# Kernel tuning notes

Hardware: AMD Instinct MI355X
Metric: run time of the kernel (lower is better)

## Reference

```python
import jax, jax.numpy as jnp
import numpy as np

N_NODES = 50000


def gcn_conv(x, edge_index, W, b, n_nodes):
    # PyG GCNConv: h = D^{-1/2} (A + I) D^{-1/2} (x @ W) + b
    loops = jnp.arange(n_nodes, dtype=edge_index.dtype)
    src = jnp.concatenate([edge_index[0], loops])
    dst = jnp.concatenate([edge_index[1], loops])
    deg = jax.ops.segment_sum(jnp.ones_like(dst, dtype=x.dtype), dst,
                              num_segments=n_nodes)
    dinv = jnp.where(deg > 0, jax.lax.rsqrt(deg), 0.0)
    norm = dinv[src] * dinv[dst]                      # [E+N]
    h = x @ W                                          # [N, out]
    msg = h[src] * norm[:, None]                       # gather + scale
    out = jax.ops.segment_sum(msg, dst, num_segments=n_nodes)
    return out + b


def setup_inputs() -> dict:
    key = jax.random.key(0)
    ks = jax.random.split(key, 8)
    in_c, hid_c, out_c = 256, 128, 64
    x = jax.random.normal(ks[0], (N_NODES, in_c), dtype=jnp.float32)
    edge_index = jax.random.randint(ks[1], (2, 800000), 0, N_NODES, dtype=jnp.int64)
    pos_edge_index = jax.random.randint(ks[2], (2, 200000), 0, N_NODES, dtype=jnp.int64)
    neg_edge_index = jax.random.randint(ks[3], (2, 200000), 0, N_NES if False else N_NODES, dtype=jnp.int64)
    W1 = jax.random.normal(ks[4], (in_c, hid_c), dtype=jnp.float32) / np.sqrt(in_c)
    b1 = jnp.zeros((hid_c,), dtype=jnp.float32)
    W2 = jax.random.normal(ks[5], (hid_c, out_c), dtype=jnp.float32) / np.sqrt(hid_c)
    b2 = jnp.zeros((out_c,), dtype=jnp.float32)
    return {"x": x, "edge_index": edge_index, "pos_edge_index": pos_edge_index,
            "neg_edge_index": neg_edge_index, "W1": W1, "b1": b1, "W2": W2, "b2": b2}


def reference(x, edge_index, pos_edge_index, neg_edge_index, W1, b1, W2, b2):
    n = x.shape[0]
    h = jax.nn.relu(gcn_conv(x, edge_index, W1, b1, n))
    z = gcn_conv(h, edge_index, W2, b2, n)             # [N, out_c]
    ei = jnp.concatenate([pos_edge_index, neg_edge_index], axis=-1)
    logits = jnp.sum(z[ei[0]] * z[ei[1]], axis=-1)     # [E_pos + E_neg]
    return logits
```

## Files before the change

### kernel.cpp

```cpp
#include <hip/hip_runtime.h>
#include <stdint.h>

constexpr int N_NODES = 50000;
constexpr int E_EDGES = 800000;
constexpr int E_PAIR  = 200000;
constexpr int C_IN    = 256;
constexpr int C_HID   = 128;
constexpr int C_OUT   = 64;
constexpr int SLOT    = 64;

constexpr int NBUCK = 49;
constexpr int BCAP  = 18432;
constexpr int CHUNK = 2048;

typedef __attribute__((ext_vector_type(8))) short bf8_t;
typedef __attribute__((ext_vector_type(4))) float f32x4;

__device__ inline void bf_split(float v, uint32_t& hi16, uint32_t& lo16) {
    union { float f; uint32_t u; } c; c.f = v;
    hi16 = c.u >> 16;
    union { uint32_t u; float f; } h; h.u = hi16 << 16;
    float r = v - h.f;
    union { float f; uint32_t u; } rr; rr.f = r;
    lo16 = rr.u >> 16;
}

__device__ inline uint16_t f2bf(float f) {
    union { float f; uint32_t u; } c; c.f = f;
    uint32_t u = c.u + 0x7fff + ((c.u >> 16) & 1);
    return (uint16_t)(u >> 16);
}
__device__ inline uint32_t pack2bf(float a, float b) {
    union { float f; uint32_t u; } ca, cb; ca.f = a; cb.f = b;
    uint32_t ua = ca.u + 0x7fff + ((ca.u >> 16) & 1);
    uint32_t ub = cb.u + 0x7fff + ((cb.u >> 16) & 1);
    return (ua >> 16) | ((ub >> 16) << 16);
}
__device__ inline void acc_bf8(float* a, uint4 v) {
    const uint32_t p[4] = {v.x, v.y, v.z, v.w};
#pragma unroll
    for (int i = 0; i < 4; ++i) {
        union { uint32_t u; float f; } lo, hi;
        lo.u = p[i] << 16; hi.u = p[i] & 0xffff0000u;
        a[2 * i]     += lo.f;
        a[2 * i + 1] += hi.f;
    }
}
__device__ inline float dot_bf8(uint4 a, uint4 b) {
    const uint32_t pa[4] = {a.x, a.y, a.z, a.w};
    const uint32_t pb[4] = {b.x, b.y, b.z, b.w};
    float v = 0.f;
#pragma unroll
    for (int i = 0; i < 4; ++i) {
        union { uint32_t u; float f; } al, ah, bl, bh;
        al.u = pa[i] << 16; ah.u = pa[i] & 0xffff0000u;
        bl.u = pb[i] << 16; bh.u = pb[i] & 0xffff0000u;
        v += al.f * bl.f + ah.f * bh.f;
    }
    return v;
}

__global__ __launch_bounds__(256) void binA_kernel(
        const int* __restrict__ src, const int* __restrict__ dst,
        int* __restrict__ gcur, uint32_t* __restrict__ ebuf) {
    __shared__ int cnt[NBUCK], loc[NBUCK], lim[NBUCK], abase[NBUCK], wcur[NBUCK];
    __shared__ uint32_t stag[CHUNK];
    __shared__ uint8_t  bof[CHUNK];

    const int t  = threadIdx.x;
    const int e0 = blockIdx.x * CHUNK;
    const int n  = min(CHUNK, E_EDGES - e0);

    if (t < NBUCK) cnt[t] = 0;
    __syncthreads();

    uint32_t pk[CHUNK / 256]; int bk[CHUNK / 256];
    int ne = 0;
    for (int j = t; j < n; j += 256) {
        int d = dst[e0 + j], s = src[e0 + j];
        int b = d >> 10;
        pk[ne] = ((uint32_t)(d & 1023) << 16) | (uint32_t)s;
        bk[ne] = b;
        atomicAdd(&cnt[b], 1);
        ++ne;
    }
    __syncthreads();
    if (t == 0) {
        int run = 0;
        for (int b = 0; b < NBUCK; ++b) { loc[b] = run; run += cnt[b]; }
    }
    __syncthreads();
    if (t < NBUCK) {
        int base = atomicAdd(&gcur[t], cnt[t]);
        int room = BCAP - base; if (room < 0) room = 0;
        lim[t]   = loc[t] + room;
        abase[t] = t * BCAP + base - loc[t];
        wcur[t]  = loc[t];
    }
    __syncthreads();
#pragma unroll
    for (int i = 0; i < CHUNK / 256; ++i) {
        if (i < ne) {
            int p = atomicAdd(&wcur[bk[i]], 1);
            stag[p] = pk[i];
            bof[p]  = (uint8_t)bk[i];
        }
    }
    __syncthreads();
    for (int j = t; j < n; j += 256) {
        int b = bof[j];
        if (j < lim[b]) ebuf[abase[b] + j] = stag[j];
    }
}

__global__ __launch_bounds__(1024) void binB_kernel(
        const int* __restrict__ gcur, const uint32_t* __restrict__ ebuf,
        uint16_t* __restrict__ col2, int* __restrict__ degc,
        float* __restrict__ dinv) {
    __shared__ int cur[1024];
    const int t = threadIdx.x;
    const int b = blockIdx.x;
    cur[t] = 0;
    __syncthreads();

    int cn = gcur[b]; if (cn > BCAP) cn = BCAP;
    const uint32_t* eb = ebuf + (size_t)b * BCAP;
    const size_t nbase = (size_t)b << 10;

    int j = t;
    for (; j + 3 * 1024 < cn; j += 4 * 1024) {
        uint32_t v0 = eb[j], v1 = eb[j + 1024], v2 = eb[j + 2048], v3 = eb[j + 3072];
        int p0 = atomicAdd(&cur[v0 >> 16], 1);
        int p1 = atomicAdd(&cur[v1 >> 16], 1);
        int p2 = atomicAdd(&cur[v2 >> 16], 1);
        int p3 = atomicAdd(&cur[v3 >> 16], 1);
        if (p0 < SLOT) col2[((nbase + (v0 >> 16)) << 6) + p0] = (uint16_t)(v0 & 0xffff);
        if (p1 < SLOT) col2[((nbase + (v1 >> 16)) << 6) + p1] = (uint16_t)(v1 & 0xffff);
        if (p2 < SLOT) col2[((nbase + (v2 >> 16)) << 6) + p2] = (uint16_t)(v2 & 0xffff);
        if (p3 < SLOT) col2[((nbase + (v3 >> 16)) << 6) + p3] = (uint16_t)(v3 & 0xffff);
    }
    for (; j < cn; j += 1024) {
        uint32_t v = eb[j];
        int p = atomicAdd(&cur[v >> 16], 1);
        if (p < SLOT) col2[((nbase + (v >> 16)) << 6) + p] = (uint16_t)(v & 0xffff);
    }
    __syncthreads();
    int node = (int)nbase + t;
    if (node < N_NODES) {
        int dg = cur[t];
        degc[node] = dg;
        dinv[node] = rsqrtf((float)dg + 1.0f);
    }
}

template<int K, int N>
__global__ void wprep_kernel(const float* __restrict__ W, uint16_t* __restrict__ swz) {
    int id = blockIdx.x * blockDim.x + threadIdx.x;
    if (id >= K * N) return;
    int k = id / N, n = id & (N - 1);
    uint32_t h, l; bf_split(W[id], h, l);
    int c = k >> 5, kq = (k >> 3) & 3, kk = k & 7, ct = n >> 4, nn = n & 15;
    int idx = (((c * (N / 16) + ct) * 4 + kq) * 16 + nn) * 8 + kk;
    swz[idx]         = (uint16_t)h;
    swz[K * N + idx] = (uint16_t)l;
}

template<int K, int N>
__global__ __launch_bounds__(256, 3) void gemm_mfma_kernel(
        const float* __restrict__ A, const uint16_t* __restrict__ Bswz,
        const float* __restrict__ dinv, uint16_t* __restrict__ out, int M) {
    constexpr int BM = 64, BK = 32;
    constexpr int CT   = N / 32;
    constexpr int NSUB = N / 16;
    constexpr int ABYTES = BM * BK * 2;
    constexpr int BBYTES = NSUB * 1024;
    __shared__ char sm[2 * ABYTES + 2 * BBYTES];
    char* As_hi = sm;
    char* As_lo = sm + ABYTES;
    char* Bs_hi = sm + 2 * ABYTES;
    char* Bs_lo = sm + 2 * ABYTES + BBYTES;

    const int t    = threadIdx.x;
    const int lane = t & 63;
    const int w    = t >> 6;
    const int wrow = w & 1, wcol = w >> 1;
    const int m0   = blockIdx.x * BM;

    const int sr = t >> 2, skq = t & 3;
    int arow = m0 + sr; if (arow > M - 1) arow = M - 1;
    const float* aptr = A + (size_t)arow * K + skq * 8;
    const int aslot = ((sr >> 4) * 64 + skq * 16 + (sr & 15)) * 16;

    f32x4 acc[2][CT];
#pragma unroll
    for (int rt = 0; rt < 2; ++rt)
#pragma unroll
        for (int ct = 0; ct < CT; ++ct) {
            f32x4 z = {0.f, 0.f, 0.f, 0.f};
            acc[rt][ct] = z;
        }

    const uint4* gh = (const uint4*)Bswz;
    const uint4* gl = (const uint4*)(Bswz + (size_t)K * N);

    constexpr int NCH = K / BK;
#pragma unroll 1
    for (int c = 0; c < NCH; ++c) {
        float4 v0 = *(const float4*)(aptr + c * BK);
        float4 v1 = *(const float4*)(aptr + c * BK + 4);
        uint4 bh0, bl0, bh1, bl1;
        {
            const uint4* ch = gh + (size_t)c * (BBYTES / 16);
            const uint4* cl = gl + (size_t)c * (BBYTES / 16);
            bh0 = ch[t]; bl0 = cl[t];
            if constexpr (NSUB == 8) { bh1 = ch[t + 256]; bl1 = cl[t + 256]; }
        }
        __syncthreads();
        {
            float e[8] = {v0.x, v0.y, v0.z, v0.w, v1.x, v1.y, v1.z, v1.w};
            uint32_t hp[4], lp[4];
#pragma unroll
            for (int j = 0; j < 4; ++j) {
                uint32_t h0, l0, h1, l1;
                bf_split(e[2 * j],     h0, l0);
                bf_split(e[2 * j + 1], h1, l1);
                hp[j] = h0 | (h1 << 16);
                lp[j] = l0 | (l1 << 16);
            }
            *(uint4*)(As_hi + aslot) = make_uint4(hp[0], hp[1], hp[2], hp[3]);
            *(uint4*)(As_lo + aslot) = make_uint4(lp[0], lp[1], lp[2], lp[3]);
        }
        *(uint4*)(Bs_hi + t * 16) = bh0;
        *(uint4*)(Bs_lo + t * 16) = bl0;
        if constexpr (NSUB == 8) {
            *(uint4*)(Bs_hi + (t + 256) * 16) = bh1;
            *(uint4*)(Bs_lo + (t + 256) * 16) = bl1;
        }
        __syncthreads();
        bf8_t Ah[2], Al[2];
#pragma unroll
        for (int rt = 0; rt < 2; ++rt) {
            int st = wrow * 2 + rt;
            Ah[rt] = *(const bf8_t*)(As_hi + st * 1024 + lane * 16);
            Al[rt] = *(const bf8_t*)(As_lo + st * 1024 + lane * 16);
        }
#pragma unroll
        for (int ct = 0; ct < CT; ++ct) {
            int cg = wcol * CT + ct;
            bf8_t Bh = *(const bf8_t*)(Bs_hi + cg * 1024 + lane * 16);
            bf8_t Bl = *(const bf8_t*)(Bs_lo + cg * 1024 + lane * 16);
#pragma unroll
            for (int rt = 0; rt < 2; ++rt) {
                acc[rt][ct] = __builtin_amdgcn_mfma_f32_16x16x32_bf16(Ah[rt], Bh, acc[rt][ct], 0, 0, 0);
                acc[rt][ct] = __builtin_amdgcn_mfma_f32_16x16x32_bf16(Ah[rt], Bl, acc[rt][ct], 0, 0, 0);
                acc[rt][ct] = __builtin_amdgcn_mfma_f32_16x16x32_bf16(Al[rt], Bh, acc[rt][ct], 0, 0, 0);
            }
        }
    }

#pragma unroll
    for (int rt = 0; rt < 2; ++rt) {
        int rowbase = m0 + wrow * 32 + rt * 16 + (lane >> 4) * 4;
#pragma unroll
        for (int ct = 0; ct < CT; ++ct) {
            int n = (wcol * CT + ct) * 16 + (lane & 15);
#pragma unroll
            for (int r = 0; r < 4; ++r) {
                int m = rowbase + r;
                if (m < M) out[(size_t)m * N + n] = f2bf(acc[rt][ct][r] * dinv[m]);
            }
        }
    }
}

__global__ __launch_bounds__(256, 3) void gemm_a16_kernel(
        const uint16_t* __restrict__ A, const uint16_t* __restrict__ Bswz,
        const float* __restrict__ dinv, uint16_t* __restrict__ out, int M) {
    constexpr int K = 128, N = 64, BM = 64, BK = 32;
    constexpr int CT = 2;
    constexpr int ABYTES = 4096, BBYTES = 4096;
    __shared__ char sm[ABYTES + 2 * BBYTES];
    char* As    = sm;
    char* Bs_hi = sm + ABYTES;
    char* Bs_lo = sm + ABYTES + BBYTES;

    const int t    = threadIdx.x;
    const int lane = t & 63;
    const int w    = t >> 6;
    const int wrow = w & 1, wcol = w >> 1;
    const int m0   = blockIdx.x * BM;

    const int sr = t >> 2, skq = t & 3;
    int arow = m0 + sr; if (arow > M - 1) arow = M - 1;
    const uint16_t* aptr = A + (size_t)arow * K + skq * 8;
    const int aslot = ((sr >> 4) * 64 + skq * 16 + (sr & 15)) * 16;

    f32x4 acc[2][CT];
#pragma unroll
    for (int rt = 0; rt < 2; ++rt)
#pragma unroll
        for (int ct = 0; ct < CT; ++ct) {
            f32x4 z = {0.f, 0.f, 0.f, 0.f};
            acc[rt][ct] = z;
        }

    const uint4* gh = (const uint4*)Bswz;
    const uint4* gl = (const uint4*)(Bswz + (size_t)K * N);

    constexpr int NCH = K / BK;
#pragma unroll 1
    for (int c = 0; c < NCH; ++c) {
        uint4 av  = *(const uint4*)(aptr + c * BK);
        uint4 bh0 = gh[(size_t)c * 256 + t];
        uint4 bl0 = gl[(size_t)c * 256 + t];
        __syncthreads();
        *(uint4*)(As + aslot)    = av;
        *(uint4*)(Bs_hi + t * 16) = bh0;
        *(uint4*)(Bs_lo + t * 16) = bl0;
        __syncthreads();
        bf8_t Ah[2];
#pragma unroll
        for (int rt = 0; rt < 2; ++rt)
            Ah[rt] = *(const bf8_t*)(As + (wrow * 2 + rt) * 1024 + lane * 16);
#pragma unroll
        for (int ct = 0; ct < CT; ++ct) {
            int cg = wcol * CT + ct;
            bf8_t Bh = *(const bf8_t*)(Bs_hi + cg * 1024 + lane * 16);
            bf8_t Bl = *(const bf8_t*)(Bs_lo + cg * 1024 + lane * 16);
#pragma unroll
            for (int rt = 0; rt < 2; ++rt) {
                acc[rt][ct] = __builtin_amdgcn_mfma_f32_16x16x32_bf16(Ah[rt], Bh, acc[rt][ct], 0, 0, 0);
                acc[rt][ct] = __builtin_amdgcn_mfma_f32_16x16x32_bf16(Ah[rt], Bl, acc[rt][ct], 0, 0, 0);
            }
        }
    }

#pragma unroll
    for (int rt = 0; rt < 2; ++rt) {
        int rowbase = m0 + wrow * 32 + rt * 16 + (lane >> 4) * 4;
#pragma unroll
        for (int ct = 0; ct < CT; ++ct) {
            int n = (wcol * CT + ct) * 16 + (lane & 15);
#pragma unroll
            for (int r = 0; r < 4; ++r) {
                int m = rowbase + r;
                if (m < M) out[(size_t)m * N + n] = f2bf(acc[rt][ct][r] * dinv[m]);
            }
        }
    }
}

template<int F, bool RELU>
__global__ __launch_bounds__(256) void gather_kernel(
        const uint16_t* __restrict__ col2, const int* __restrict__ degc,
        const uint16_t* __restrict__ hs, const float* __restrict__ dinv,
        const float* __restrict__ bias, uint16_t* __restrict__ out) {
    constexpr int LPN = F / 8;
    constexpr int NPW = 64 / LPN;
    const int lane = threadIdx.x & 63;
    const int sub  = lane / LPN;
    const int l    = lane % LPN;
    const int node = blockIdx.x * (4 * NPW) + (threadIdx.x >> 6) * NPW + sub;
    if (node >= N_NODES) return;

    int dg = degc[node]; if (dg > SLOT) dg = SLOT;
    const uint4* hs4 = (const uint4*)hs;

    float a0[8], a1[8];
    {
        uint4 self = hs4[(size_t)node * LPN + l];
#pragma unroll
        for (int i = 0; i < 8; ++i) { a0[i] = 0.f; a1[i] = 0.f; }
        acc_bf8(a0, self);
    }
    const int base = node * SLOT;

    for (int c = 0; c * LPN < dg; ++c) {
        int cnt = dg - c * LPN; if (cnt > LPN) cnt = LPN;
        int cv = (l < cnt) ? (int)col2[base + c * LPN + l] : 0;
        int j = 0;
        for (; j + 4 <= cnt; j += 4) {
            int s0 = __shfl(cv, sub * LPN + j,     64);
            int s1 = __shfl(cv, sub * LPN + j + 1, 64);
            int s2 = __shfl(cv, sub * LPN + j + 2, 64);
            int s3 = __shfl(cv, sub * LPN + j + 3, 64);
            uint4 v0 = hs4[(size_t)s0 * LPN + l];
            uint4 v1 = hs4[(size_t)s1 * LPN + l];
            uint4 v2 = hs4[(size_t)s2 * LPN + l];
            uint4 v3 = hs4[(size_t)s3 * LPN + l];
            acc_bf8(a0, v0); acc_bf8(a1, v1);
            acc_bf8(a0, v2); acc_bf8(a1, v3);
        }
        for (; j < cnt; ++j) {
            int s = __shfl(cv, sub * LPN + j, 64);
            uint4 v = hs4[(size_t)s * LPN + l];
            acc_bf8(a0, v);
        }
    }

    const float dn = dinv[node];
    float4 bb0 = ((const float4*)bias)[2 * l];
    float4 bb1 = ((const float4*)bias)[2 * l + 1];
    float o[8];
    o[0] = (a0[0] + a1[0]) * dn + bb0.x;
    o[1] = (a0[1] + a1[1]) * dn + bb0.y;
    o[2] = (a0[2] + a1[2]) * dn + bb0.z;
    o[3] = (a0[3] + a1[3]) * dn + bb0.w;
    o[4] = (a0[4] + a1[4]) * dn + bb1.x;
    o[5] = (a0[5] + a1[5]) * dn + bb1.y;
    o[6] = (a0[6] + a1[6]) * dn + bb1.z;
    o[7] = (a0[7] + a1[7]) * dn + bb1.w;
    if (RELU) {
#pragma unroll
        for (int i = 0; i < 8; ++i) o[i] = fmaxf(o[i], 0.f);
    }
    uint4 res = make_uint4(pack2bf(o[0], o[1]), pack2bf(o[2], o[3]),
                           pack2bf(o[4], o[5]), pack2bf(o[6], o[7]));
    ((uint4*)out)[(size_t)node * LPN + l] = res;
}

__global__ __launch_bounds__(256) void logits_kernel(
        const int* __restrict__ pos, const int* __restrict__ neg,
        const uint16_t* __restrict__ z, float* __restrict__ out) {
    const int t = threadIdx.x;
    const int l = t & 7;
    const int e = (blockIdx.x * 256 + t) >> 3;
    if (e >= 2 * E_PAIR) return;
    int s, d;
    if (e < E_PAIR) { s = pos[e];          d = pos[E_PAIR + e]; }
    else            { s = neg[e - E_PAIR]; d = neg[e];          }
    const uint4* z4 = (const uint4*)z;
    uint4 ua = z4[(size_t)s * 8 + l];
    uint4 ub = z4[(size_t)d * 8 + l];
    float v = dot_bf8(ua, ub);
    v += __shfl_xor(v, 1, 64);
    v += __shfl_xor(v, 2, 64);
    v += __shfl_xor(v, 4, 64);
    if (l == 0) out[e] = v;
}

extern "C" void kernel_launch(void* const* d_in, const int* in_sizes, int n_in,
                              void* d_out, int out_size, void* d_ws, size_t ws_size,
                              hipStream_t stream) {
    const float* x   = (const float*)d_in[0];
    const int*   ei  = (const int*)d_in[1];
    const int*   pos = (const int*)d_in[2];
    const int*   neg = (const int*)d_in[3];
    const float* W1  = (const float*)d_in[4];
    const float* b1  = (const float*)d_in[5];
    const float* W2  = (const float*)d_in[6];
    const float* b2  = (const float*)d_in[7];
    float* out = (float*)d_out;

    const int* src = ei;
    const int* dst = ei + E_EDGES;

    char* ws = (char*)d_ws;
    int*      degc  = (int*)ws;
    float*    dinv  = (float*)(ws + 200704);
    uint16_t* col2  = (uint16_t*)(ws + 401408);
    int*      gcur  = (int*)(ws + 6801408);
    uint16_t* B1swz = (uint16_t*)(ws + 6802432);
    uint16_t* B2swz = (uint16_t*)(ws + 6933504);
    uint16_t* h0s   = (uint16_t*)(ws + 6966272);
    uint16_t* h     = (uint16_t*)(ws + 19766272);
    uint16_t* z0s   = (uint16_t*)(ws + 32566272);
    uint16_t* zbuf  = (uint16_t*)(ws + 38966272);
    uint32_t* ebuf  = (uint32_t*)(ws + 45366272);

    wprep_kernel<C_IN, C_HID><<<(C_IN * C_HID + 255) / 256, 256, 0, stream>>>(W1, B1swz);
    wprep_kernel<C_HID, C_OUT><<<(C_HID * C_OUT + 255) / 256, 256, 0, stream>>>(W2, B2swz);

    hipMemsetAsync(gcur, 0, NBUCK * sizeof(int), stream);
    binA_kernel<<<(E_EDGES + CHUNK - 1) / CHUNK, 256, 0, stream>>>(src, dst, gcur, ebuf);
    binB_kernel<<<NBUCK, 1024, 0, stream>>>(gcur, ebuf, col2, degc, dinv);

    gemm_mfma_kernel<C_IN, C_HID><<<(N_NODES + 63) / 64, 256, 0, stream>>>(
        x, B1swz, dinv, h0s, N_NODES);

    gather_kernel<C_HID, true><<<N_NODES / 16, 256, 0, stream>>>(
        col2, degc, h0s, dinv, b1, h);

    gemm_a16_kernel<<<(N_NODES + 63) / 64, 256, 0, stream>>>(
        h, B2swz, dinv, z0s, N_NODES);
    gather_kernel<C_OUT, false><<<(N_NODES + 31) / 32, 256, 0, stream>>>(
        col2, degc, z0s, dinv, b2, zbuf);

    logits_kernel<<<(2 * E_PAIR * 8 + 255) / 256, 256, 0, stream>>>(pos, neg, zbuf, out);
}
```

Baseline: 222.3 us.

## Fuse layer-1 gather with layer-2 GEMM and merge weight prep kernels

Merges the first-layer neighbor aggregation (with bias and ReLU) and the second-layer 128x64 MFMA GEMM into one kernel. Each block aggregates 16 nodes into LDS and then multiplies them by the swizzled W2 directly, so the intermediate hidden matrix no longer makes a round trip through global memory. It also folds the two weight-swizzle kernels and the counter memset into a single prep kernel to save launches. The cost is that each 16-row GEMM tile reads B from global memory with no reuse across blocks.

```diff
diff --git a/kernel.cpp b/kernel.cpp
--- a/kernel.cpp
+++ b/kernel.cpp
@@ -58,6 +58,32 @@
         v += al.f * bl.f + ah.f * bh.f;
     }
     return v;
+}
+
+template<int N>
+__device__ inline int wswz_idx(int k, int n) {
+    int c = k >> 5, kq = (k >> 3) & 3, kk = k & 7, ct = n >> 4, nn = n & 15;
+    return (((c * (N / 16) + ct) * 4 + kq) * 16 + nn) * 8 + kk;
+}
+
+__global__ __launch_bounds__(256) void prep_kernel(
+        const float* __restrict__ W1, const float* __restrict__ W2,
+        uint16_t* __restrict__ s1, uint16_t* __restrict__ s2,
+        int* __restrict__ gcur) {
+    int id = blockIdx.x * 256 + threadIdx.x;
+    if (id < NBUCK) gcur[id] = 0;
+    if (id < C_IN * C_HID) {
+        uint32_t h, l; bf_split(W1[id], h, l);
+        int idx = wswz_idx<C_HID>(id / C_HID, id & (C_HID - 1));
+        s1[idx]                 = (uint16_t)h;
+        s1[C_IN * C_HID + idx]  = (uint16_t)l;
+    } else if (id < C_IN * C_HID + C_HID * C_OUT) {
+        int id2 = id - C_IN * C_HID;
+        uint32_t h, l; bf_split(W2[id2], h, l);
+        int idx = wswz_idx<C_OUT>(id2 / C_OUT, id2 & (C_OUT - 1));
+        s2[idx]                 = (uint16_t)h;
+        s2[C_HID * C_OUT + idx] = (uint16_t)l;
+    }
 }
 
 __global__ __launch_bounds__(256) void binA_kernel(
@@ -151,18 +177,6 @@
         degc[node] = dg;
         dinv[node] = rsqrtf((float)dg + 1.0f);
     }
-}
-
-template<int K, int N>
-__global__ void wprep_kernel(const float* __restrict__ W, uint16_t* __restrict__ swz) {
-    int id = blockIdx.x * blockDim.x + threadIdx.x;
-    if (id >= K * N) return;
-    int k = id / N, n = id & (N - 1);
-    uint32_t h, l; bf_split(W[id], h, l);
-    int c = k >> 5, kq = (k >> 3) & 3, kk = k & 7, ct = n >> 4, nn = n & 15;
-    int idx = (((c * (N / 16) + ct) * 4 + kq) * 16 + nn) * 8 + kk;
-    swz[idx]         = (uint16_t)h;
-    swz[K * N + idx] = (uint16_t)l;
 }
 
 template<int K, int N>
@@ -273,80 +287,88 @@
     }
 }
 
-__global__ __launch_bounds__(256, 3) void gemm_a16_kernel(
-        const uint16_t* __restrict__ A, const uint16_t* __restrict__ Bswz,
-        const float* __restrict__ dinv, uint16_t* __restrict__ out, int M) {
-    constexpr int K = 128, N = 64, BM = 64, BK = 32;
-    constexpr int CT = 2;
-    constexpr int ABYTES = 4096, BBYTES = 4096;
-    __shared__ char sm[ABYTES + 2 * BBYTES];
-    char* As    = sm;
-    char* Bs_hi = sm + ABYTES;
-    char* Bs_lo = sm + ABYTES + BBYTES;
-
+__global__ __launch_bounds__(256) void gather_gemm_kernel(
+        const uint16_t* __restrict__ col2, const int* __restrict__ degc,
+        const uint16_t* __restrict__ h0s, const float* __restrict__ dinv,
+        const float* __restrict__ bias, const uint16_t* __restrict__ B2swz,
+        uint16_t* __restrict__ z0s) {
+    __shared__ uint4 hlds[256];
     const int t    = threadIdx.x;
     const int lane = t & 63;
     const int w    = t >> 6;
-    const int wrow = w & 1, wcol = w >> 1;
-    const int m0   = blockIdx.x * BM;
-
-    const int sr = t >> 2, skq = t & 3;
-    int arow = m0 + sr; if (arow > M - 1) arow = M - 1;
-    const uint16_t* aptr = A + (size_t)arow * K + skq * 8;
-    const int aslot = ((sr >> 4) * 64 + skq * 16 + (sr & 15)) * 16;
-
-    f32x4 acc[2][CT];
-#pragma unroll
-    for (int rt = 0; rt < 2; ++rt)
-#pragma unroll
-        for (int ct = 0; ct < CT; ++ct) {
-            f32x4 z = {0.f, 0.f, 0.f, 0.f};
-            acc[rt][ct] = z;
-        }
-
-    const uint4* gh = (const uint4*)Bswz;
-    const uint4* gl = (const uint4*)(Bswz + (size_t)K * N);
-
-    constexpr int NCH = K / BK;
-#pragma unroll 1
-    for (int c = 0; c < NCH; ++c) {
-        uint4 av  = *(const uint4*)(aptr + c * BK);
-        uint4 bh0 = gh[(size_t)c * 256 + t];
-        uint4 bl0 = gl[(size_t)c * 256 + t];
-        __syncthreads();
-        *(uint4*)(As + aslot)    = av;
-        *(uint4*)(Bs_hi + t * 16) = bh0;
-        *(uint4*)(Bs_lo + t * 16) = bl0;
-        __syncthreads();
-        bf8_t Ah[2];
-#pragma unroll
-        for (int rt = 0; rt < 2; ++rt)
-            Ah[rt] = *(const bf8_t*)(As + (wrow * 2 + rt) * 1024 + lane * 16);
-#pragma unroll
-        for (int ct = 0; ct < CT; ++ct) {
-            int cg = wcol * CT + ct;
-            bf8_t Bh = *(const bf8_t*)(Bs_hi + cg * 1024 + lane * 16);
-            bf8_t Bl = *(const bf8_t*)(Bs_lo + cg * 1024 + lane * 16);
-#pragma unroll
-            for (int rt = 0; rt < 2; ++rt) {
-                acc[rt][ct] = __builtin_amdgcn_mfma_f32_16x16x32_bf16(Ah[rt], Bh, acc[rt][ct], 0, 0, 0);
-                acc[rt][ct] = __builtin_amdgcn_mfma_f32_16x16x32_bf16(Ah[rt], Bl, acc[rt][ct], 0, 0, 0);
-            }
-        }
-    }
-
-#pragma unroll
-    for (int rt = 0; rt < 2; ++rt) {
-        int rowbase = m0 + wrow * 32 + rt * 16 + (lane >> 4) * 4;
-#pragma unroll
-        for (int ct = 0; ct < CT; ++ct) {
-            int n = (wcol * CT + ct) * 16 + (lane & 15);
-#pragma unroll
-            for (int r = 0; r < 4; ++r) {
-                int m = rowbase + r;
-                if (m < M) out[(size_t)m * N + n] = f2bf(acc[rt][ct][r] * dinv[m]);
-            }
-        }
+    const int sub  = lane >> 4;
+    const int l    = lane & 15;
+    const int node_loc = w * 4 + sub;
+    const int node = blockIdx.x * 16 + node_loc;
+
+    int dg = degc[node]; if (dg > SLOT) dg = SLOT;
+    const uint4* hs4 = (const uint4*)h0s;
+    float a0[8], a1[8];
+    {
+        uint4 self = hs4[(size_t)node * 16 + l];
+#pragma unroll
+        for (int i = 0; i < 8; ++i) { a0[i] = 0.f; a1[i] = 0.f; }
+        acc_bf8(a0, self);
+    }
+    const int base = node * SLOT;
+    for (int c = 0; c * 16 < dg; ++c) {
+        int cnt = dg - c * 16; if (cnt > 16) cnt = 16;
+        int cv = (l < cnt) ? (int)col2[base + c * 16 + l] : 0;
+        int j = 0;
+        for (; j + 4 <= cnt; j += 4) {
+            int s0 = __shfl(cv, sub * 16 + j,     64);
+            int s1 = __shfl(cv, sub * 16 + j + 1, 64);
+            int s2 = __shfl(cv, sub * 16 + j + 2, 64);
+            int s3 = __shfl(cv, sub * 16 + j + 3, 64);
+            uint4 v0 = hs4[(size_t)s0 * 16 + l];
+            uint4 v1 = hs4[(size_t)s1 * 16 + l];
+            uint4 v2 = hs4[(size_t)s2 * 16 + l];
+            uint4 v3 = hs4[(size_t)s3 * 16 + l];
+            acc_bf8(a0, v0); acc_bf8(a1, v1);
+            acc_bf8(a0, v2); acc_bf8(a1, v3);
+        }
+        for (; j < cnt; ++j) {
+            int s = __shfl(cv, sub * 16 + j, 64);
+            uint4 v = hs4[(size_t)s * 16 + l];
+            acc_bf8(a0, v);
+        }
+    }
+    {
+        const float dn = dinv[node];
+        float4 bb0 = ((const float4*)bias)[2 * l];
+        float4 bb1 = ((const float4*)bias)[2 * l + 1];
+        float o[8];
+        o[0] = fmaxf((a0[0] + a1[0]) * dn + bb0.x, 0.f);
+        o[1] = fmaxf((a0[1] + a1[1]) * dn + bb0.y, 0.f);
+        o[2] = fmaxf((a0[2] + a1[2]) * dn + bb0.z, 0.f);
+        o[3] = fmaxf((a0[3] + a1[3]) * dn + bb0.w, 0.f);
+        o[4] = fmaxf((a0[4] + a1[4]) * dn + bb1.x, 0.f);
+        o[5] = fmaxf((a0[5] + a1[5]) * dn + bb1.y, 0.f);
+        o[6] = fmaxf((a0[6] + a1[6]) * dn + bb1.z, 0.f);
+        o[7] = fmaxf((a0[7] + a1[7]) * dn + bb1.w, 0.f);
+        hlds[l * 16 + node_loc] = make_uint4(
+            pack2bf(o[0], o[1]), pack2bf(o[2], o[3]),
+            pack2bf(o[4], o[5]), pack2bf(o[6], o[7]));
+    }
+    __syncthreads();
+
+    f32x4 acc = {0.f, 0.f, 0.f, 0.f};
+    const char* hb = (const char*)hlds;
+#pragma unroll
+    for (int c = 0; c < 4; ++c) {
+        bf8_t Af = *(const bf8_t*)(hb + c * 1024 + lane * 16);
+        const uint16_t* bp = B2swz + (c * 4 + w) * 512 + lane * 8;
+        bf8_t Bh = *(const bf8_t*)bp;
+        bf8_t Bl = *(const bf8_t*)(bp + C_HID * C_OUT);
+        acc = __builtin_amdgcn_mfma_f32_16x16x32_bf16(Af, Bh, acc, 0, 0, 0);
+        acc = __builtin_amdgcn_mfma_f32_16x16x32_bf16(Af, Bl, acc, 0, 0, 0);
+    }
+    const int colg = w * 16 + (lane & 15);
+    const int rowb = blockIdx.x * 16 + (lane >> 4) * 4;
+#pragma unroll
+    for (int r = 0; r < 4; ++r) {
+        int m = rowb + r;
+        z0s[(size_t)m * C_OUT + colg] = f2bf(acc[r] * dinv[m]);
     }
 }
 
@@ -463,26 +485,22 @@
     uint16_t* B1swz = (uint16_t*)(ws + 6802432);
     uint16_t* B2swz = (uint16_t*)(ws + 6933504);
     uint16_t* h0s   = (uint16_t*)(ws + 6966272);
-    uint16_t* h     = (uint16_t*)(ws + 19766272);
     uint16_t* z0s   = (uint16_t*)(ws + 32566272);
     uint16_t* zbuf  = (uint16_t*)(ws + 38966272);
     uint32_t* ebuf  = (uint32_t*)(ws + 45366272);
 
-    wprep_kernel<C_IN, C_HID><<<(C_IN * C_HID + 255) / 256, 256, 0, stream>>>(W1, B1swz);
-    wprep_kernel<C_HID, C_OUT><<<(C_HID * C_OUT + 255) / 256, 256, 0, stream>>>(W2, B2swz);
-
-    hipMemsetAsync(gcur, 0, NBUCK * sizeof(int), stream);
+    prep_kernel<<<(C_IN * C_HID + C_HID * C_OUT + 255) / 256, 256, 0, stream>>>(
+        W1, W2, B1swz, B2swz, gcur);
+
     binA_kernel<<<(E_EDGES + CHUNK - 1) / CHUNK, 256, 0, stream>>>(src, dst, gcur, ebuf);
     binB_kernel<<<NBUCK, 1024, 0, stream>>>(gcur, ebuf, col2, degc, dinv);
 
     gemm_mfma_kernel<C_IN, C_HID><<<(N_NODES + 63) / 64, 256, 0, stream>>>(
         x, B1swz, dinv, h0s, N_NODES);
 
-    gather_kernel<C_HID, true><<<N_NODES / 16, 256, 0, stream>>>(
-        col2, degc, h0s, dinv, b1, h);
-
-    gemm_a16_kernel<<<(N_NODES + 63) / 64, 256, 0, stream>>>(
-        h, B2swz, dinv, z0s, N_NODES);
+    gather_gemm_kernel<<<N_NODES / 16, 256, 0, stream>>>(
+        col2, degc, h0s, dinv, b1, B2swz, z0s);
+
     gather_kernel<C_OUT, false><<<(N_NODES + 31) / 32, 256, 0, stream>>>(
         col2, degc, z0s, dinv, b2, zbuf);
 
```

Result: faster. 206.3 us (-7.2%).
